# Performance work log

Hardware: AMD Instinct MI355X
Metric: run time of the kernel (lower is better)

## Reference

```python
import jax, jax.numpy as jnp
import numpy as np
import math

NEG_INF = -1e9  # large negative used as masked-logit value (pre-scaling, as in the original)


def setup_inputs() -> dict:
    key = jax.random.key(0)
    k1, k2, k3 = jax.random.split(key, 3)
    bs, ql, kl, d = 8, 2048, 2048, 512
    return {
        "query": jax.random.normal(k1, (bs, ql, d), dtype=jnp.float32),
        "key": jax.random.normal(k2, (bs, kl, d), dtype=jnp.float32),
        "value": jax.random.normal(k3, (bs, kl, d), dtype=jnp.float32),
        "use_mask": 1,
        "cell_dim": 512,
    }


def reference(query, key, value, use_mask, cell_dim):
    bs, ql, d = query.shape[0], query.shape[1], value.shape[2]
    kl = key.shape[1]
    # [bs, ql, kl] raw scores
    mm = jnp.einsum("bqd,bkd->bqk", query, key)
    if use_mask:
        # mask positions where key index > query index (strictly future)
        q_idx = jnp.arange(ql)[:, None]
        k_idx = jnp.arange(kl)[None, :]
        mask = (k_idx > q_idx).astype(mm.dtype)  # [ql, kl]
        mm = mm + mask[None, :, :] * NEG_INF
    # log_softmax(...).exp() == softmax, computed stably in one pass
    w = jax.nn.softmax(mm / math.sqrt(cell_dim), axis=2)
    # weighted value aggregation (original broadcasts to [bs,ql,kl,d]; einsum fuses it)
    res = jnp.einsum("bqk,bkd->bqd", w, value)
    return res
```

## Files before the change

### kernel.cpp

```cpp
#include <hip/hip_runtime.h>
#include <math.h>

typedef __bf16 bf16x8 __attribute__((ext_vector_type(8)));
typedef float floatx4 __attribute__((ext_vector_type(4)));
typedef unsigned short ushort8_t __attribute__((ext_vector_type(8)));

#define BSZ 8
#define SEQ 2048
#define DIM 512
#define BKEY 32
#define BQ 32

__device__ __forceinline__ unsigned short f2bf(float f) {
    unsigned int u = __float_as_uint(f);
    u += 0x7fffu + ((u >> 16) & 1u);
    return (unsigned short)(u >> 16);
}
__device__ __forceinline__ float bf2f(unsigned short s) {
    return __uint_as_float(((unsigned int)s) << 16);
}

#define ASYNC16(g, l) __builtin_amdgcn_global_load_lds( \
    (const __attribute__((address_space(1))) unsigned int*)(g), \
    (__attribute__((address_space(3))) unsigned int*)(l), 16, 0, 0)

__global__ __launch_bounds__(256) void conv_k(const float* __restrict__ K,
                                              unsigned short* __restrict__ Kb) {
    size_t i = ((size_t)blockIdx.x * 256 + threadIdx.x) * 8;
    float4 a = *(const float4*)(K + i);
    float4 b = *(const float4*)(K + i + 4);
    ushort8_t u;
    u[0]=f2bf(a.x); u[1]=f2bf(a.y); u[2]=f2bf(a.z); u[3]=f2bf(a.w);
    u[4]=f2bf(b.x); u[5]=f2bf(b.y); u[6]=f2bf(b.z); u[7]=f2bf(b.w);
    *(ushort8_t*)(Kb + i) = u;
}

__global__ __launch_bounds__(256) void trans_v(const float* __restrict__ V,
                                               unsigned short* __restrict__ Vt) {
    __shared__ unsigned short T[BKEY][DIM + 8];
    const int bid = blockIdx.x;
    const int b = bid & 7, kb = bid >> 3;
    const float* src = V + ((size_t)b * SEQ + (size_t)kb * BKEY) * DIM;
    const int tid = threadIdx.x;
    #pragma unroll
    for (int i = 0; i < 16; ++i) {
        const int idx = i * 256 + tid;
        const int key = idx >> 7;
        const int d = (idx & 127) * 4;
        float4 x = *(const float4*)(src + (size_t)key * DIM + d);
        T[key][d]   = f2bf(x.x);
        T[key][d+1] = f2bf(x.y);
        T[key][d+2] = f2bf(x.z);
        T[key][d+3] = f2bf(x.w);
    }
    __syncthreads();
    unsigned short* dst = Vt + (size_t)(b * (SEQ / BKEY) + kb) * DIM * BKEY;
    #pragma unroll
    for (int i = 0; i < 8; ++i) {
        const int cidx = i * 256 + tid;
        const int d = cidx >> 2;
        const int kc = cidx & 3;
        ushort8_t v;
        #pragma unroll
        for (int k2 = 0; k2 < 8; ++k2) v[k2] = T[kc * 8 + k2][d];
        *(ushort8_t*)(dst + cidx * 8) = v;
    }
}


template <int SPLIT>
__global__ __launch_bounds__(128, 2)
void attn_fwd(const float* __restrict__ Q,
              const unsigned short* __restrict__ Kb,
              const unsigned short* __restrict__ Vt,
              unsigned short* __restrict__ PartO,
              float* __restrict__ Pml,
              float* __restrict__ O)
{
    __shared__ unsigned short Ksh[BKEY * DIM];
    __shared__ unsigned short Vsh[DIM * BKEY];
    __shared__ unsigned short Psh[2 * 16 * BKEY];

    const int tid  = threadIdx.x;
    const int lane = tid & 63;
    const int wv   = tid >> 6;
    const int ml   = lane & 15;
    const int quad = lane >> 4;

    const int bid = blockIdx.x;
    const int b   = bid & 7;
    const int j   = bid >> 3;
    int t, c;
    if (SPLIT) {
        if (j < 64)       { t = 63 - (j >> 2); c = j & 3; }
        else if (j < 112) { int u = j - 64; int q3 = u / 3; t = 47 - q3; c = u - q3 * 3; }
        else if (j < 144) { int u = j - 112; t = 31 - (u >> 1); c = u & 1; }
        else              { t = 159 - j; c = 0; }
    } else { t = 63 - j; c = 0; }
    const int kt0 = c * 16;
    const int kt1 = min(kt0 + 16, t + 1);
    const bool is_split = SPLIT && (t >= 16);
    const int q0 = t * BQ;

    const float* Qb = Q + (size_t)b * SEQ * DIM;
    const unsigned short* Kbb = Kb + (size_t)b * SEQ * DIM;
    const unsigned short* Vtb = Vt + (size_t)b * SEQ * DIM;
    float* Ob = O + (size_t)b * SEQ * DIM;

    bf16x8 qf[16];
    {
        const float* qp = Qb + (size_t)(q0 + wv * 16 + ml) * DIM + quad * 8;
        #pragma unroll
        for (int kc = 0; kc < 16; ++kc) {
            float4 x = *(const float4*)(qp + kc * 32);
            float4 y = *(const float4*)(qp + kc * 32 + 4);
            union { bf16x8 v; unsigned short s[8]; } u;
            u.s[0]=f2bf(x.x); u.s[1]=f2bf(x.y); u.s[2]=f2bf(x.z); u.s[3]=f2bf(x.w);
            u.s[4]=f2bf(y.x); u.s[5]=f2bf(y.y); u.s[6]=f2bf(y.z); u.s[7]=f2bf(y.w);
            qf[kc] = u.v;
        }
    }

    floatx4 acc[32];
    #pragma unroll
    for (int i = 0; i < 32; ++i) acc[i] = (floatx4){0.f, 0.f, 0.f, 0.f};
    float mrun[4] = {-INFINITY, -INFINITY, -INFINITY, -INFINITY};
    float lrun[4] = {0.f, 0.f, 0.f, 0.f};

    const float CS = 1.4426950408889634f * 0.04419417382415922f;

    for (int kt = kt0; kt < kt1; ++kt) {
        const int k0 = kt * BKEY;

        __syncthreads();

        const unsigned short* Kt = Kbb + (size_t)k0 * DIM;
        #pragma unroll
        for (int i = 0; i < 16; ++i) {
            const int ci  = i * 128 + tid;
            const int row = ci >> 6;
            const int ch  = (ci & 63) ^ (row & 7);
            ASYNC16(Kt + (size_t)row * DIM + ch * 8, &Ksh[ci * 8]);
        }
        const unsigned short* Vtile = Vtb + (size_t)kt * (DIM * BKEY);
        #pragma unroll
        for (int i = 0; i < 16; ++i) {
            const int ci = i * 128 + tid;
            const int d  = ci >> 2;
            const int kc = (ci & 3) ^ (d & 3);
            ASYNC16(Vtile + d * BKEY + kc * 8, &Vsh[ci * 8]);
        }
        __syncthreads();

        floatx4 s0 = (floatx4){0,0,0,0}, s1 = (floatx4){0,0,0,0};
        floatx4 s0b = (floatx4){0,0,0,0}, s1b = (floatx4){0,0,0,0};
        const int sw = ml & 7;
        #pragma unroll
        for (int kc = 0; kc < 16; kc += 2) {
            const int ch0 = kc * 4 + quad, ch1 = (kc + 1) * 4 + quad;
            bf16x8 a0 = *(bf16x8*)&Ksh[ml * DIM + ((ch0 ^ sw) << 3)];
            bf16x8 a1 = *(bf16x8*)&Ksh[(16 + ml) * DIM + ((ch0 ^ sw) << 3)];
            bf16x8 b0 = *(bf16x8*)&Ksh[ml * DIM + ((ch1 ^ sw) << 3)];
            bf16x8 b1 = *(bf16x8*)&Ksh[(16 + ml) * DIM + ((ch1 ^ sw) << 3)];
            s0  = __builtin_amdgcn_mfma_f32_16x16x32_bf16(qf[kc],     a0, s0,  0, 0, 0);
            s1  = __builtin_amdgcn_mfma_f32_16x16x32_bf16(qf[kc],     a1, s1,  0, 0, 0);
            s0b = __builtin_amdgcn_mfma_f32_16x16x32_bf16(qf[kc + 1], b0, s0b, 0, 0, 0);
            s1b = __builtin_amdgcn_mfma_f32_16x16x32_bf16(qf[kc + 1], b1, s1b, 0, 0, 0);
        }
        s0 = s0 + s0b;
        s1 = s1 + s1b;

        float z[2][4], pr[2][4], al[4], rs[4];
        if (kt == t) {
            #pragma unroll
            for (int r = 0; r < 4; ++r) {
                const int qg = q0 + wv * 16 + quad * 4 + r;
                z[0][r] = (k0 + ml > qg)      ? -INFINITY : s0[r] * CS;
                z[1][r] = (k0 + 16 + ml > qg) ? -INFINITY : s1[r] * CS;
            }
        } else {
            #pragma unroll
            for (int r = 0; r < 4; ++r) { z[0][r] = s0[r] * CS; z[1][r] = s1[r] * CS; }
        }
        #pragma unroll
        for (int r = 0; r < 4; ++r) {
            float v = fmaxf(z[0][r], z[1][r]);
            v = fmaxf(v, __shfl_xor(v, 1, 64));
            v = fmaxf(v, __shfl_xor(v, 2, 64));
            v = fmaxf(v, __shfl_xor(v, 4, 64));
            v = fmaxf(v, __shfl_xor(v, 8, 64));
            const float nm = fmaxf(mrun[r], v);
            al[r]   = __builtin_amdgcn_exp2f(mrun[r] - nm);
            mrun[r] = nm;
        }
        #pragma unroll
        for (int r = 0; r < 4; ++r) {
            pr[0][r] = __builtin_amdgcn_exp2f(z[0][r] - mrun[r]);
            pr[1][r] = __builtin_amdgcn_exp2f(z[1][r] - mrun[r]);
            float s = pr[0][r] + pr[1][r];
            s += __shfl_xor(s, 1, 64);
            s += __shfl_xor(s, 2, 64);
            s += __shfl_xor(s, 4, 64);
            s += __shfl_xor(s, 8, 64);
            rs[r] = s;
        }
        #pragma unroll
        for (int r = 0; r < 4; ++r) lrun[r] = lrun[r] * al[r] + rs[r];

        if (al[0] < 1.f || al[1] < 1.f || al[2] < 1.f || al[3] < 1.f) {
            #pragma unroll
            for (int nt = 0; nt < 32; ++nt) {
                acc[nt][0] *= al[0]; acc[nt][1] *= al[1];
                acc[nt][2] *= al[2]; acc[nt][3] *= al[3];
            }
        }

        unsigned short* Pw = &Psh[wv * (16 * BKEY)];
        #pragma unroll
        for (int nt = 0; nt < 2; ++nt) {
            #pragma unroll
            for (int r = 0; r < 4; ++r) {
                const int row = quad * 4 + r, col = nt * 16 + ml;
                Pw[row * BKEY + ((((col >> 3) ^ (row & 3)) << 3) | (col & 7))] = f2bf(pr[nt][r]);
            }
        }
        asm volatile("s_waitcnt lgkmcnt(0)" ::: "memory");
        bf16x8 pf = *(bf16x8*)&Pw[ml * BKEY + ((quad ^ (ml & 3)) << 3)];

        #pragma unroll
        for (int nt = 0; nt < 32; ++nt) {
            const int drow = nt * 16 + ml;
            bf16x8 vf = *(bf16x8*)&Vsh[drow * BKEY + ((quad ^ (drow & 3)) << 3)];
            acc[nt] = __builtin_amdgcn_mfma_f32_16x16x32_bf16(pf, vf, acc[nt], 0, 0, 0);
        }
    }

    if (!is_split) {
        float inv[4];
        #pragma unroll
        for (int r = 0; r < 4; ++r) inv[r] = 1.f / lrun[r];
        #pragma unroll
        for (int nt = 0; nt < 32; ++nt) {
            #pragma unroll
            for (int r = 0; r < 4; ++r) {
                const int row = q0 + wv * 16 + quad * 4 + r;
                Ob[(size_t)row * DIM + nt * 16 + ml] = acc[nt][r] * inv[r];
            }
        }
    } else {
        const size_t slot = (size_t)(b * 144 + j);
        unsigned short* po = PartO + slot * (BQ * DIM);
        #pragma unroll
        for (int nt = 0; nt < 32; ++nt) {
            #pragma unroll
            for (int r = 0; r < 4; ++r) {
                const int prow = wv * 16 + quad * 4 + r;
                po[prow * DIM + nt * 16 + ml] = f2bf(acc[nt][r]);
            }
        }
        if (ml == 0) {
            #pragma unroll
            for (int r = 0; r < 4; ++r) {
                const int prow = wv * 16 + quad * 4 + r;
                Pml[slot * 64 + prow * 2]     = mrun[r];
                Pml[slot * 64 + prow * 2 + 1] = lrun[r];
            }
        }
    }
}

__global__ __launch_bounds__(256)
void attn_merge(const unsigned short* __restrict__ PartO,
                const float* __restrict__ Pml,
                float* __restrict__ O)
{
    const int bid = blockIdx.x;
    const int b = bid & 7;
    const int t = 16 + (bid >> 3);
    const int nc = (t >> 4) + 1;
    int j0;
    if (t >= 48)      j0 = (63 - t) * 4;
    else if (t >= 32) j0 = 64 + (47 - t) * 3;
    else              j0 = 112 + (31 - t) * 2;

    const int r  = threadIdx.x >> 3;
    const int d0 = (threadIdx.x & 7) * 64;

    float m[4], l[4];
    float M = -INFINITY;
    for (int cc = 0; cc < nc; ++cc) {
        const size_t slot = (size_t)(b * 144 + j0 + cc);
        m[cc] = Pml[slot * 64 + r * 2];
        l[cc] = Pml[slot * 64 + r * 2 + 1];
        M = fmaxf(M, m[cc]);
    }
    float L = 0.f;
    for (int cc = 0; cc < nc; ++cc) L += l[cc] * __builtin_amdgcn_exp2f(m[cc] - M);

    float o[64];
    #pragma unroll
    for (int i = 0; i < 64; ++i) o[i] = 0.f;
    for (int cc = 0; cc < nc; ++cc) {
        const size_t slot = (size_t)(b * 144 + j0 + cc);
        const float w = __builtin_amdgcn_exp2f(m[cc] - M);
        const unsigned short* po = PartO + slot * (BQ * DIM) + (size_t)r * DIM + d0;
        #pragma unroll
        for (int i = 0; i < 8; ++i) {
            ushort8_t v = *(const ushort8_t*)(po + i * 8);
            #pragma unroll
            for (int k2 = 0; k2 < 8; ++k2) o[i * 8 + k2] += w * bf2f(v[k2]);
        }
    }
    const float invL = 1.f / L;
    float* out = O + ((size_t)b * SEQ + (size_t)t * BQ + r) * DIM + d0;
    #pragma unroll
    for (int i = 0; i < 16; ++i) {
        float4 v4 = { o[i*4] * invL, o[i*4+1] * invL, o[i*4+2] * invL, o[i*4+3] * invL };
        *(float4*)(out + i * 4) = v4;
    }
}

extern "C" void kernel_launch(void* const* d_in, const int* in_sizes, int n_in,
                              void* d_out, int out_size, void* d_ws, size_t ws_size,
                              hipStream_t stream) {
    const float* Q = (const float*)d_in[0];
    const float* K = (const float*)d_in[1];
    const float* V = (const float*)d_in[2];
    float* Out = (float*)d_out;

    const size_t elems = (size_t)BSZ * SEQ * DIM;
    unsigned short* Kb = (unsigned short*)d_ws;
    unsigned short* Vt = Kb + elems;
    unsigned short* PartO = Vt + elems;
    float* Pml = (float*)(PartO + (size_t)BSZ * 144 * BQ * DIM);

    const size_t need_split = 2 * elems * 2
                            + (size_t)BSZ * 144 * BQ * DIM * 2
                            + (size_t)BSZ * 144 * 64 * 4;
    conv_k<<<dim3(elems / 8 / 256), dim3(256), 0, stream>>>(K, Kb);
    trans_v<<<dim3(BSZ * (SEQ / BKEY)), dim3(256), 0, stream>>>(V, Vt);

    if (ws_size >= need_split) {
        attn_fwd<1><<<dim3(BSZ * 160), dim3(128), 0, stream>>>(Q, Kb, Vt, PartO, Pml, Out);
        attn_merge<<<dim3(BSZ * 48), dim3(256), 0, stream>>>(PartO, Pml, Out);
    } else {
        attn_fwd<0><<<dim3(BSZ * 64), dim3(128), 0, stream>>>(Q, Kb, Vt, PartO, Pml, Out);
    }
}
```

Before: 355.6 us.

## Double query tile to 64 rows with 4 waves sharing K/V tiles

Raises the query block from 32 to 64 rows and runs 256 threads (4 waves) per block, so each K/V tile loaded into LDS is reused by twice as many query rows. The causal split schedule, merge indexing and partial buffers are rescaled to match. The K conversion and V transpose are fused into a single prepass launch, and the per-wave P handoff now uses a block barrier instead of a waitcnt. In exchange there are half as many attention blocks, which risks lower occupancy, plus an extra block-wide sync in every key iteration. The QK accumulation also drops its dual accumulator chains, which lengthens the MFMA dependency chain.

```diff
diff --git a/kernel.cpp b/kernel.cpp
--- a/kernel.cpp
+++ b/kernel.cpp
@@ -9,7 +9,8 @@
 #define SEQ 2048
 #define DIM 512
 #define BKEY 32
-#define BQ 32
+#define BQ 64
+#define NEGB -1.0e30f
 
 __device__ __forceinline__ unsigned short f2bf(float f) {
     unsigned int u = __float_as_uint(f);
@@ -24,52 +25,52 @@
     (const __attribute__((address_space(1))) unsigned int*)(g), \
     (__attribute__((address_space(3))) unsigned int*)(l), 16, 0, 0)
 
-__global__ __launch_bounds__(256) void conv_k(const float* __restrict__ K,
-                                              unsigned short* __restrict__ Kb) {
-    size_t i = ((size_t)blockIdx.x * 256 + threadIdx.x) * 8;
-    float4 a = *(const float4*)(K + i);
-    float4 b = *(const float4*)(K + i + 4);
-    ushort8_t u;
-    u[0]=f2bf(a.x); u[1]=f2bf(a.y); u[2]=f2bf(a.z); u[3]=f2bf(a.w);
-    u[4]=f2bf(b.x); u[5]=f2bf(b.y); u[6]=f2bf(b.z); u[7]=f2bf(b.w);
-    *(ushort8_t*)(Kb + i) = u;
-}
-
-__global__ __launch_bounds__(256) void trans_v(const float* __restrict__ V,
+__global__ __launch_bounds__(256) void prepass(const float* __restrict__ K,
+                                               const float* __restrict__ V,
+                                               unsigned short* __restrict__ Kb,
                                                unsigned short* __restrict__ Vt) {
     __shared__ unsigned short T[BKEY][DIM + 8];
-    const int bid = blockIdx.x;
-    const int b = bid & 7, kb = bid >> 3;
-    const float* src = V + ((size_t)b * SEQ + (size_t)kb * BKEY) * DIM;
-    const int tid = threadIdx.x;
-    #pragma unroll
-    for (int i = 0; i < 16; ++i) {
-        const int idx = i * 256 + tid;
-        const int key = idx >> 7;
-        const int d = (idx & 127) * 4;
-        float4 x = *(const float4*)(src + (size_t)key * DIM + d);
-        T[key][d]   = f2bf(x.x);
-        T[key][d+1] = f2bf(x.y);
-        T[key][d+2] = f2bf(x.z);
-        T[key][d+3] = f2bf(x.w);
-    }
-    __syncthreads();
-    unsigned short* dst = Vt + (size_t)(b * (SEQ / BKEY) + kb) * DIM * BKEY;
-    #pragma unroll
-    for (int i = 0; i < 8; ++i) {
-        const int cidx = i * 256 + tid;
-        const int d = cidx >> 2;
-        const int kc = cidx & 3;
-        ushort8_t v;
-        #pragma unroll
-        for (int k2 = 0; k2 < 8; ++k2) v[k2] = T[kc * 8 + k2][d];
-        *(ushort8_t*)(dst + cidx * 8) = v;
+    const int j = blockIdx.x, tid = threadIdx.x;
+    if (j < 4096) {
+        size_t i = ((size_t)j * 256 + tid) * 8;
+        float4 a = *(const float4*)(K + i);
+        float4 b = *(const float4*)(K + i + 4);
+        ushort8_t u;
+        u[0]=f2bf(a.x); u[1]=f2bf(a.y); u[2]=f2bf(a.z); u[3]=f2bf(a.w);
+        u[4]=f2bf(b.x); u[5]=f2bf(b.y); u[6]=f2bf(b.z); u[7]=f2bf(b.w);
+        *(ushort8_t*)(Kb + i) = u;
+    } else {
+        const int bid = j - 4096;
+        const int b = bid & 7, kb = bid >> 3;
+        const float* src = V + ((size_t)b * SEQ + (size_t)kb * BKEY) * DIM;
+        #pragma unroll
+        for (int i = 0; i < 16; ++i) {
+            const int idx = i * 256 + tid;
+            const int key = idx >> 7;
+            const int d = (idx & 127) * 4;
+            float4 x = *(const float4*)(src + (size_t)key * DIM + d);
+            T[key][d]   = f2bf(x.x);
+            T[key][d+1] = f2bf(x.y);
+            T[key][d+2] = f2bf(x.z);
+            T[key][d+3] = f2bf(x.w);
+        }
+        __syncthreads();
+        unsigned short* dst = Vt + (size_t)(b * (SEQ / BKEY) + kb) * DIM * BKEY;
+        #pragma unroll
+        for (int i = 0; i < 8; ++i) {
+            const int cidx = i * 256 + tid;
+            const int d = cidx >> 2, kc = cidx & 3;
+            ushort8_t v;
+            #pragma unroll
+            for (int k2 = 0; k2 < 8; ++k2) v[k2] = T[kc * 8 + k2][d];
+            *(ushort8_t*)(dst + cidx * 8) = v;
+        }
     }
 }
 
 
 template <int SPLIT>
-__global__ __launch_bounds__(128, 2)
+__global__ __launch_bounds__(256, 2)
 void attn_fwd(const float* __restrict__ Q,
               const unsigned short* __restrict__ Kb,
               const unsigned short* __restrict__ Vt,
@@ -79,7 +80,7 @@
 {
     __shared__ unsigned short Ksh[BKEY * DIM];
     __shared__ unsigned short Vsh[DIM * BKEY];
-    __shared__ unsigned short Psh[2 * 16 * BKEY];
+    __shared__ unsigned short Psh[4 * 16 * BKEY];
 
     const int tid  = threadIdx.x;
     const int lane = tid & 63;
@@ -92,15 +93,15 @@
     const int j   = bid >> 3;
     int t, c;
     if (SPLIT) {
-        if (j < 64)       { t = 63 - (j >> 2); c = j & 3; }
-        else if (j < 112) { int u = j - 64; int q3 = u / 3; t = 47 - q3; c = u - q3 * 3; }
-        else if (j < 144) { int u = j - 112; t = 31 - (u >> 1); c = u & 1; }
-        else              { t = 159 - j; c = 0; }
-    } else { t = 63 - j; c = 0; }
+        if (j < 32)      { t = 31 - (j >> 2); c = j & 3; }
+        else if (j < 56) { int u = j - 32; int q3 = u / 3; t = 23 - q3; c = u - q3 * 3; }
+        else if (j < 72) { int u = j - 56; t = 15 - (u >> 1); c = u & 1; }
+        else             { t = 7 - (j - 72); c = 0; }
+    } else { t = 31 - j; c = 0; }
     const int kt0 = c * 16;
-    const int kt1 = min(kt0 + 16, t + 1);
-    const bool is_split = SPLIT && (t >= 16);
-    const int q0 = t * BQ;
+    const int kt1 = SPLIT ? min(kt0 + 16, 2 * t + 2) : (2 * t + 2);
+    const bool is_split = SPLIT && (t >= 8);
+    const int qw = t * BQ + wv * 16;
 
     const float* Qb = Q + (size_t)b * SEQ * DIM;
     const unsigned short* Kbb = Kb + (size_t)b * SEQ * DIM;
@@ -109,7 +110,7 @@
 
     bf16x8 qf[16];
     {
-        const float* qp = Qb + (size_t)(q0 + wv * 16 + ml) * DIM + quad * 8;
+        const float* qp = Qb + (size_t)(qw + ml) * DIM + quad * 8;
         #pragma unroll
         for (int kc = 0; kc < 16; ++kc) {
             float4 x = *(const float4*)(qp + kc * 32);
@@ -124,7 +125,7 @@
     floatx4 acc[32];
     #pragma unroll
     for (int i = 0; i < 32; ++i) acc[i] = (floatx4){0.f, 0.f, 0.f, 0.f};
-    float mrun[4] = {-INFINITY, -INFINITY, -INFINITY, -INFINITY};
+    float mrun[4] = {NEGB, NEGB, NEGB, NEGB};
     float lrun[4] = {0.f, 0.f, 0.f, 0.f};
 
     const float CS = 1.4426950408889634f * 0.04419417382415922f;
@@ -136,16 +137,16 @@
 
         const unsigned short* Kt = Kbb + (size_t)k0 * DIM;
         #pragma unroll
-        for (int i = 0; i < 16; ++i) {
-            const int ci  = i * 128 + tid;
+        for (int i = 0; i < 8; ++i) {
+            const int ci  = i * 256 + tid;
             const int row = ci >> 6;
             const int ch  = (ci & 63) ^ (row & 7);
             ASYNC16(Kt + (size_t)row * DIM + ch * 8, &Ksh[ci * 8]);
         }
         const unsigned short* Vtile = Vtb + (size_t)kt * (DIM * BKEY);
         #pragma unroll
-        for (int i = 0; i < 16; ++i) {
-            const int ci = i * 128 + tid;
+        for (int i = 0; i < 8; ++i) {
+            const int ci = i * 256 + tid;
             const int d  = ci >> 2;
             const int kc = (ci & 3) ^ (d & 3);
             ASYNC16(Vtile + d * BKEY + kc * 8, &Vsh[ci * 8]);
@@ -153,30 +154,23 @@
         __syncthreads();
 
         floatx4 s0 = (floatx4){0,0,0,0}, s1 = (floatx4){0,0,0,0};
-        floatx4 s0b = (floatx4){0,0,0,0}, s1b = (floatx4){0,0,0,0};
         const int sw = ml & 7;
         #pragma unroll
-        for (int kc = 0; kc < 16; kc += 2) {
-            const int ch0 = kc * 4 + quad, ch1 = (kc + 1) * 4 + quad;
-            bf16x8 a0 = *(bf16x8*)&Ksh[ml * DIM + ((ch0 ^ sw) << 3)];
-            bf16x8 a1 = *(bf16x8*)&Ksh[(16 + ml) * DIM + ((ch0 ^ sw) << 3)];
-            bf16x8 b0 = *(bf16x8*)&Ksh[ml * DIM + ((ch1 ^ sw) << 3)];
-            bf16x8 b1 = *(bf16x8*)&Ksh[(16 + ml) * DIM + ((ch1 ^ sw) << 3)];
-            s0  = __builtin_amdgcn_mfma_f32_16x16x32_bf16(qf[kc],     a0, s0,  0, 0, 0);
-            s1  = __builtin_amdgcn_mfma_f32_16x16x32_bf16(qf[kc],     a1, s1,  0, 0, 0);
-            s0b = __builtin_amdgcn_mfma_f32_16x16x32_bf16(qf[kc + 1], b0, s0b, 0, 0, 0);
-            s1b = __builtin_amdgcn_mfma_f32_16x16x32_bf16(qf[kc + 1], b1, s1b, 0, 0, 0);
-        }
-        s0 = s0 + s0b;
-        s1 = s1 + s1b;
+        for (int kc = 0; kc < 16; ++kc) {
+            const int ch = kc * 4 + quad;
+            bf16x8 kf0 = *(bf16x8*)&Ksh[ml * DIM + ((ch ^ sw) << 3)];
+            bf16x8 kf1 = *(bf16x8*)&Ksh[(16 + ml) * DIM + ((ch ^ sw) << 3)];
+            s0 = __builtin_amdgcn_mfma_f32_16x16x32_bf16(qf[kc], kf0, s0, 0, 0, 0);
+            s1 = __builtin_amdgcn_mfma_f32_16x16x32_bf16(qf[kc], kf1, s1, 0, 0, 0);
+        }
 
         float z[2][4], pr[2][4], al[4], rs[4];
-        if (kt == t) {
-            #pragma unroll
-            for (int r = 0; r < 4; ++r) {
-                const int qg = q0 + wv * 16 + quad * 4 + r;
-                z[0][r] = (k0 + ml > qg)      ? -INFINITY : s0[r] * CS;
-                z[1][r] = (k0 + 16 + ml > qg) ? -INFINITY : s1[r] * CS;
+        if (kt >= 2 * t) {
+            #pragma unroll
+            for (int r = 0; r < 4; ++r) {
+                const int qg = qw + quad * 4 + r;
+                z[0][r] = (k0 + ml > qg)      ? NEGB : s0[r] * CS;
+                z[1][r] = (k0 + 16 + ml > qg) ? NEGB : s1[r] * CS;
             }
         } else {
             #pragma unroll
@@ -208,11 +202,9 @@
         for (int r = 0; r < 4; ++r) lrun[r] = lrun[r] * al[r] + rs[r];
 
         if (al[0] < 1.f || al[1] < 1.f || al[2] < 1.f || al[3] < 1.f) {
-            #pragma unroll
-            for (int nt = 0; nt < 32; ++nt) {
-                acc[nt][0] *= al[0]; acc[nt][1] *= al[1];
-                acc[nt][2] *= al[2]; acc[nt][3] *= al[3];
-            }
+            const floatx4 alv = (floatx4){al[0], al[1], al[2], al[3]};
+            #pragma unroll
+            for (int nt = 0; nt < 32; ++nt) acc[nt] = acc[nt] * alv;
         }
 
         unsigned short* Pw = &Psh[wv * (16 * BKEY)];
@@ -224,7 +216,7 @@
                 Pw[row * BKEY + ((((col >> 3) ^ (row & 3)) << 3) | (col & 7))] = f2bf(pr[nt][r]);
             }
         }
-        asm volatile("s_waitcnt lgkmcnt(0)" ::: "memory");
+        __syncthreads();
         bf16x8 pf = *(bf16x8*)&Pw[ml * BKEY + ((quad ^ (ml & 3)) << 3)];
 
         #pragma unroll
@@ -243,27 +235,27 @@
         for (int nt = 0; nt < 32; ++nt) {
             #pragma unroll
             for (int r = 0; r < 4; ++r) {
-                const int row = q0 + wv * 16 + quad * 4 + r;
+                const int row = qw + quad * 4 + r;
                 Ob[(size_t)row * DIM + nt * 16 + ml] = acc[nt][r] * inv[r];
             }
         }
     } else {
-        const size_t slot = (size_t)(b * 144 + j);
+        const size_t slot = (size_t)(b * 72 + j);
         unsigned short* po = PartO + slot * (BQ * DIM);
         #pragma unroll
         for (int nt = 0; nt < 32; ++nt) {
             #pragma unroll
             for (int r = 0; r < 4; ++r) {
                 const int prow = wv * 16 + quad * 4 + r;
-                po[prow * DIM + nt * 16 + ml] = f2bf(acc[nt][r]);
+                po[(size_t)prow * DIM + nt * 16 + ml] = f2bf(acc[nt][r]);
             }
         }
         if (ml == 0) {
             #pragma unroll
             for (int r = 0; r < 4; ++r) {
                 const int prow = wv * 16 + quad * 4 + r;
-                Pml[slot * 64 + prow * 2]     = mrun[r];
-                Pml[slot * 64 + prow * 2 + 1] = lrun[r];
+                Pml[slot * 128 + prow * 2]     = mrun[r];
+                Pml[slot * 128 + prow * 2 + 1] = lrun[r];
             }
         }
     }
@@ -274,41 +266,51 @@
                 const float* __restrict__ Pml,
                 float* __restrict__ O)
 {
-    const int bid = blockIdx.x;
-    const int b = bid & 7;
-    const int t = 16 + (bid >> 3);
-    const int nc = (t >> 4) + 1;
+    const int bid  = blockIdx.x;
+    const int b    = bid & 7;
+    const int rest = bid >> 3;
+    const int t    = 8 + (rest >> 1);
+    const int half = rest & 1;
+    const int nc   = t / 8 + 1;
     int j0;
-    if (t >= 48)      j0 = (63 - t) * 4;
-    else if (t >= 32) j0 = 64 + (47 - t) * 3;
-    else              j0 = 112 + (31 - t) * 2;
-
-    const int r  = threadIdx.x >> 3;
+    if (t >= 24)      j0 = (31 - t) * 4;
+    else if (t >= 16) j0 = 32 + (23 - t) * 3;
+    else              j0 = 56 + (15 - t) * 2;
+
+    const int r  = half * 32 + (threadIdx.x >> 3);
     const int d0 = (threadIdx.x & 7) * 64;
 
     float m[4], l[4];
-    float M = -INFINITY;
-    for (int cc = 0; cc < nc; ++cc) {
-        const size_t slot = (size_t)(b * 144 + j0 + cc);
-        m[cc] = Pml[slot * 64 + r * 2];
-        l[cc] = Pml[slot * 64 + r * 2 + 1];
-        M = fmaxf(M, m[cc]);
+    float M = NEGB;
+    #pragma unroll
+    for (int cc = 0; cc < 4; ++cc) {
+        if (cc < nc) {
+            const size_t slot = (size_t)(b * 72 + j0 + cc);
+            m[cc] = Pml[slot * 128 + r * 2];
+            l[cc] = Pml[slot * 128 + r * 2 + 1];
+            M = fmaxf(M, m[cc]);
+        }
     }
     float L = 0.f;
-    for (int cc = 0; cc < nc; ++cc) L += l[cc] * __builtin_amdgcn_exp2f(m[cc] - M);
+    #pragma unroll
+    for (int cc = 0; cc < 4; ++cc)
+        if (cc < nc) L += l[cc] * __builtin_amdgcn_exp2f(m[cc] - M);
 
     float o[64];
     #pragma unroll
     for (int i = 0; i < 64; ++i) o[i] = 0.f;
-    for (int cc = 0; cc < nc; ++cc) {
-        const size_t slot = (size_t)(b * 144 + j0 + cc);
-        const float w = __builtin_amdgcn_exp2f(m[cc] - M);
-        const unsigned short* po = PartO + slot * (BQ * DIM) + (size_t)r * DIM + d0;
-        #pragma unroll
-        for (int i = 0; i < 8; ++i) {
-            ushort8_t v = *(const ushort8_t*)(po + i * 8);
-            #pragma unroll
-            for (int k2 = 0; k2 < 8; ++k2) o[i * 8 + k2] += w * bf2f(v[k2]);
+    #pragma unroll
+    for (int cc = 0; cc < 4; ++cc) {
+        if (cc < nc) {
+            const size_t slot = (size_t)(b * 72 + j0 + cc);
+            const float w = __builtin_amdgcn_exp2f(m[cc] - M);
+            const unsigned short* po = PartO + slot * (BQ * DIM) + (size_t)r * DIM + d0;
+            #pragma unroll
+            for (int i = 0; i < 8; ++i) {
+                ushort8_t v = *(const ushort8_t*)(po + i * 8);
+                #pragma unroll
+                for (int k2 = 0; k2 < 8; ++k2) o[i * 8 + k2] += w * bf2f(v[k2]);
+            }
         }
     }
     const float invL = 1.f / L;
@@ -332,18 +334,18 @@
     unsigned short* Kb = (unsigned short*)d_ws;
     unsigned short* Vt = Kb + elems;
     unsigned short* PartO = Vt + elems;
-    float* Pml = (float*)(PartO + (size_t)BSZ * 144 * BQ * DIM);
+    float* Pml = (float*)(PartO + (size_t)BSZ * 72 * BQ * DIM);
 
     const size_t need_split = 2 * elems * 2
-                            + (size_t)BSZ * 144 * BQ * DIM * 2
-                            + (size_t)BSZ * 144 * 64 * 4;
-    conv_k<<<dim3(elems / 8 / 256), dim3(256), 0, stream>>>(K, Kb);
-    trans_v<<<dim3(BSZ * (SEQ / BKEY)), dim3(256), 0, stream>>>(V, Vt);
+                            + (size_t)BSZ * 72 * BQ * DIM * 2
+                            + (size_t)BSZ * 72 * 128 * 4;
+
+    prepass<<<dim3(4096 + 512), dim3(256), 0, stream>>>(K, V, Kb, Vt);
 
     if (ws_size >= need_split) {
-        attn_fwd<1><<<dim3(BSZ * 160), dim3(128), 0, stream>>>(Q, Kb, Vt, PartO, Pml, Out);
+        attn_fwd<1><<<dim3(BSZ * 80), dim3(256), 0, stream>>>(Q, Kb, Vt, PartO, Pml, Out);
         attn_merge<<<dim3(BSZ * 48), dim3(256), 0, stream>>>(PartO, Pml, Out);
     } else {
-        attn_fwd<0><<<dim3(BSZ * 64), dim3(128), 0, stream>>>(Q, Kb, Vt, PartO, Pml, Out);
-    }
-}
+        attn_fwd<0><<<dim3(BSZ * 32), dim3(256), 0, stream>>>(Q, Kb, Vt, PartO, Pml, Out);
+    }
+}
```

Result: slower. 387.5 us (+9.0%).
